# Kernel tuning notes

Measured on AMD Instinct MI355X. Metric: run time of the kernel, lower is better.

Reference implementation:

```python
import jax, jax.numpy as jnp
import numpy as np

B, N, H, NH = 8, 1024, 512, 8
HD = H // NH
SCALE = float(np.sqrt(HD))


def setup_inputs() -> dict:
    key = jax.random.key(0)
    ks = jax.random.split(key, 14)
    s = 0.02
    return {
        "x": jax.random.normal(ks[0], (B, N, H), jnp.float32),
        "distance_matrix": jax.random.uniform(ks[1], (B, N, N), jnp.float32),
        "mask": jax.random.randint(ks[2], (B, N), 0, 2).astype(bool),
        "Wq": jax.random.normal(ks[3], (H, H), jnp.float32) * s,
        "bq": jnp.zeros((H,), jnp.float32),
        "Wk": jax.random.normal(ks[4], (H, H), jnp.float32) * s,
        "bk": jnp.zeros((H,), jnp.float32),
        "Wv": jax.random.normal(ks[5], (H, H), jnp.float32) * s,
        "bv": jnp.zeros((H,), jnp.float32),
        "Wo": jax.random.normal(ks[6], (H, H), jnp.float32) * s,
        "bo": jnp.zeros((H,), jnp.float32),
        "dist_emb": jax.random.normal(ks[7], (50, NH), jnp.float32) * s,
        "attn_bias": jnp.zeros((NH, 1, 1), jnp.float32),
    }


def reference(x, distance_matrix, mask, Wq, bq, Wk, bk, Wv, bv, Wo, bo, dist_emb, attn_bias):
    Bb, Nn, _ = x.shape
    # projections (torch Linear: x @ W.T + b), split heads -> [B, N, NH, HD]
    Q = (x @ Wq.T + bq).reshape(Bb, Nn, NH, HD)
    K = (x @ Wk.T + bk).reshape(Bb, Nn, NH, HD)
    V = (x @ Wv.T + bv).reshape(Bb, Nn, NH, HD)
    # scores [B, NH, N, N]
    scores = jnp.einsum('bqhd,bkhd->bhqk', Q, K) / SCALE
    # distance-bin bias lookup: [B,N,N] -> bins -> [B,N,N,NH] -> [B,NH,N,N]
    bins = jnp.clip((distance_matrix * 10.0).astype(jnp.int32), 0, 49)
    dbias = jnp.transpose(dist_emb[bins], (0, 3, 1, 2))
    scores = scores + dbias + attn_bias[None]  # attn_bias [NH,1,1] broadcasts
    scores = jnp.where(mask[:, None, None, :], -1e9, scores)  # mask over keys
    attn = jax.nn.softmax(scores, axis=-1)  # dropout = identity in eval
    out = jnp.einsum('bhqk,bkhd->bqhd', attn, V).reshape(Bb, Nn, H)
    return out @ Wo.T + bo
```

## Files before the change

### kernel.cpp

```cpp
#include <hip/hip_runtime.h>
#include <hip/hip_bf16.h>
#include <math.h>

#define B_  8
#define N_  1024
#define H_  512
#define NH_ 8
#define HD_ 64

typedef __attribute__((ext_vector_type(8))) short short8;
typedef __attribute__((ext_vector_type(4))) short short4_t;
typedef __attribute__((ext_vector_type(4))) float floatx4;

#define GPTR(p) ((const __attribute__((address_space(1))) void*)(p))
#define LPTR(p) ((__attribute__((address_space(3))) void*)(p))

#define TRB16(dst, addr, IMM) \
    asm volatile("ds_read_b64_tr_b16 %0, %1 offset:" IMM \
                 : "=v"(dst) : "v"(addr) : "memory")

#define EXP2(x) exp2f(x)
#define LOG2E 1.44269504088896f

static __device__ __forceinline__ unsigned short f2bf(float f) {
    __hip_bfloat16 h = __float2bfloat16(f);
    unsigned short u;
    __builtin_memcpy(&u, &h, 2);
    return u;
}

__global__ __launch_bounds__(256) void prep_kernel(
    const float* __restrict__ x,  const float* __restrict__ wq,
    const float* __restrict__ wk, const float* __restrict__ wv,
    const float* __restrict__ wo, unsigned short* __restrict__ dst,
    const float* __restrict__ dist, const int* __restrict__ mask,
    unsigned char* __restrict__ bins)
{
    const int bid = blockIdx.x;
    if (bid < 1280) {
        const int n4 = (4194304 + 4 * 262144) / 4;
        int i = bid * 256 + threadIdx.x;
        for (; i < n4; i += 1280 * 256) {
            const int e = i * 4;
            const float* src;
            if (e < 4194304) {
                src = x + e;
            } else {
                const int rel = e - 4194304;
                const int w = rel >> 18;
                const int off = rel & 262143;
                src = (w == 0 ? wq : w == 1 ? wk : w == 2 ? wv : wo) + off;
            }
            const float4 v = *(const float4*)src;
            ushort4 r;
            r.x = f2bf(v.x); r.y = f2bf(v.y); r.z = f2bf(v.z); r.w = f2bf(v.w);
            *(ushort4*)(dst + e) = r;
        }
    } else {
        const int gid = (bid - 1280) * 256 + threadIdx.x;
        const size_t e = (size_t)gid * 16;
        const int b = gid >> 16;
        const int k = (gid & 63) * 16;
        const float* dsrc = dist + e;
        const int*   msrc = mask + b * N_ + k;
        unsigned w[4];
        #pragma unroll
        for (int i = 0; i < 4; ++i) {
            const float4 v = *(const float4*)(dsrc + 4 * i);
            const int4  mm = *(const int4*)(msrc + 4 * i);
            int b0 = (int)(v.x * 10.f); b0 = b0 < 0 ? 0 : (b0 > 49 ? 49 : b0);
            int b1 = (int)(v.y * 10.f); b1 = b1 < 0 ? 0 : (b1 > 49 ? 49 : b1);
            int b2 = (int)(v.z * 10.f); b2 = b2 < 0 ? 0 : (b2 > 49 ? 49 : b2);
            int b3 = (int)(v.w * 10.f); b3 = b3 < 0 ? 0 : (b3 > 49 ? 49 : b3);
            if (mm.x) b0 = 255;
            if (mm.y) b1 = 255;
            if (mm.z) b2 = 255;
            if (mm.w) b3 = 255;
            w[i] = (unsigned)b0 | ((unsigned)b1 << 8) | ((unsigned)b2 << 16) | ((unsigned)b3 << 24);
        }
        uint4 u; u.x = w[0]; u.y = w[1]; u.z = w[2]; u.w = w[3];
        *(uint4*)(bins + e) = u;
    }
}

template <int BF16OUT>
static __device__ __forceinline__ void gemm_core(
    const unsigned short* __restrict__ A, const unsigned short* __restrict__ W,
    const float* __restrict__ bias, void* __restrict__ C,
    int Ncols, int K, float scale, int row0, int col0)
{
    __shared__ unsigned short As[128 * 32];
    __shared__ unsigned short Bs[128 * 32];

    const int t    = threadIdx.x;
    const int lane = t & 63;
    const int wave = t >> 6;
    const int wr   = wave >> 1;
    const int wc   = wave & 1;
    const int l15  = lane & 15;
    const int lhi  = lane >> 4;

    const int srow = wave * 32 + (lane >> 2);
    const int sk   = (lane & 3) * 8;
    const unsigned short* gA = A + (size_t)(row0 + srow) * K + sk;
    const unsigned short* gB = W + (size_t)(col0 + srow) * K + sk;

    floatx4 acc[4][4];
    #pragma unroll
    for (int m = 0; m < 4; ++m)
        #pragma unroll
        for (int n = 0; n < 4; ++n) acc[m][n] = (floatx4)0.f;

    for (int k0 = 0; k0 < K; k0 += 32) {
        __syncthreads();
        #pragma unroll
        for (int i = 0; i < 2; ++i) {
            __builtin_amdgcn_global_load_lds(GPTR(gA + (size_t)(i * 16) * K + k0),
                                             LPTR(&As[(wave * 32 + i * 16) * 32]), 16, 0, 0);
            __builtin_amdgcn_global_load_lds(GPTR(gB + (size_t)(i * 16) * K + k0),
                                             LPTR(&Bs[(wave * 32 + i * 16) * 32]), 16, 0, 0);
        }
        __syncthreads();

        short8 af[4], bf[4];
        #pragma unroll
        for (int m = 0; m < 4; ++m)
            af[m] = *(const short8*)&As[(wr * 64 + m * 16 + l15) * 32 + lhi * 8];
        #pragma unroll
        for (int n = 0; n < 4; ++n)
            bf[n] = *(const short8*)&Bs[(wc * 64 + n * 16 + l15) * 32 + lhi * 8];
        #pragma unroll
        for (int m = 0; m < 4; ++m)
            #pragma unroll
            for (int n = 0; n < 4; ++n)
                acc[m][n] = __builtin_amdgcn_mfma_f32_16x16x32_bf16(af[m], bf[n], acc[m][n], 0, 0, 0);
    }

    #pragma unroll
    for (int n = 0; n < 4; ++n) {
        const int col = col0 + wc * 64 + n * 16 + l15;
        const float bvv = bias[col];
        #pragma unroll
        for (int m = 0; m < 4; ++m) {
            #pragma unroll
            for (int r = 0; r < 4; ++r) {
                const int row = row0 + wr * 64 + m * 16 + lhi * 4 + r;
                const float v = (acc[m][n][r] + bvv) * scale;
                if (BF16OUT)
                    ((unsigned short*)C)[(size_t)row * Ncols + col] = f2bf(v);
                else
                    ((float*)C)[(size_t)row * Ncols + col] = v;
            }
        }
    }
}

__global__ __launch_bounds__(256) void gemm_qkv(
    const unsigned short* __restrict__ xb,
    const unsigned short* __restrict__ Wq, const unsigned short* __restrict__ Wk,
    const unsigned short* __restrict__ Wv,
    const float* __restrict__ bq, const float* __restrict__ bk,
    const float* __restrict__ bv,
    unsigned short* __restrict__ Qb, unsigned short* __restrict__ Kb,
    unsigned short* __restrict__ Vb)
{
    const int z = blockIdx.z;
    const unsigned short* W = z == 0 ? Wq : (z == 1 ? Wk : Wv);
    const float* bias       = z == 0 ? bq : (z == 1 ? bk : bv);
    unsigned short* C       = z == 0 ? Qb : (z == 1 ? Kb : Vb);
    const float scale       = z == 0 ? (0.125f * LOG2E) : 1.0f;
    gemm_core<1>(xb, W, bias, C, H_, H_, scale, blockIdx.y * 128, blockIdx.x * 128);
}

__global__ __launch_bounds__(256) void gemm_out(
    const unsigned short* __restrict__ Ab, const unsigned short* __restrict__ Wo,
    const float* __restrict__ bo, float* __restrict__ out)
{
    gemm_core<0>(Ab, Wo, bo, out, H_, H_, 1.0f, blockIdx.y * 128, blockIdx.x * 128);
}

__global__ __launch_bounds__(256) void attn_mfma(
    const unsigned short* __restrict__ Qg, const unsigned short* __restrict__ Kg,
    const unsigned short* __restrict__ Vg, const unsigned char* __restrict__ bins,
    const float* __restrict__ demb, const float* __restrict__ abias,
    unsigned short* __restrict__ O)
{
    const int lin = blockIdx.x + 16 * blockIdx.y + 128 * blockIdx.z;
    const int swz = (lin & 7) * 128 + (lin >> 3);
    const int qt = swz & 15;
    const int h  = (swz >> 4) & 7;
    const int b  = swz >> 7;
    const int q0 = qt * 64;
    const int t  = threadIdx.x;
    const int lane = t & 63;
    const int wave = t >> 6;
    const int l15 = lane & 15;
    const int lhi = lane >> 4;

    __shared__ unsigned short Ks[64 * 64];
    __shared__ unsigned short Vs[64 * 64];
    __shared__ unsigned short QPs[64 * 64];
    __shared__ unsigned char  Bs[64 * 80];

    float dbl = -1.442695e9f;
    if (lane < 50) dbl = (demb[lane * NH_ + h] + abias[h]) * LOG2E;

    const unsigned short* ksrc[2];
    const unsigned short* vsrc[2];
    #pragma unroll
    for (int i = 0; i < 2; ++i) {
        const int C = wave * 128 + i * 64 + lane;
        const int kr = C >> 3, c = C & 7;
        ksrc[i] = Kg + ((size_t)(b * N_) + kr) * H_ + h * HD_ + ((c ^ (kr & 7)) * 8);
        const int vd16 = C >> 7, rem = C & 127;
        const int krhi = rem >> 3, r2 = rem & 7;
        const int vkr = krhi * 4 + (r2 >> 1), vc = r2 & 1;
        vsrc[i] = Vg + ((size_t)(b * N_) + vkr) * H_ + h * HD_ + vd16 * 16 + vc * 8;
    }
    const unsigned char* bsrc = bins + ((size_t)(b * N_) + q0 + (t >> 2)) * N_ + (t & 3) * 16;
    const int bidx = (t >> 2) * 80 + (t & 3) * 16;

    {
        const int qr = t >> 2;
        const int d0 = (t & 3) * 16;
        const unsigned short* src = Qg + ((size_t)(b * N_ + q0 + qr)) * H_ + h * HD_ + d0;
        #pragma unroll
        for (int cc = 0; cc < 2; ++cc) {
            const uint4 v = *(const uint4*)(src + 8 * cc);
            const int idx = (qr * 64 + d0 + 8 * cc) ^ ((qr & 7) << 3);
            *(uint4*)&QPs[idx] = v;
        }
    }
    __syncthreads();

    short8 aq[2];
    {
        const int qrow = (wave << 4) + l15;
        #pragma unroll
        for (int ck = 0; ck < 2; ++ck) {
            const int kb = lhi * 8 + 32 * ck;
            const int idx = (qrow * 64 + kb) ^ ((qrow & 7) << 3);
            aq[ck] = *(const short8*)&QPs[idx];
        }
    }
    __syncthreads();

    unsigned short* const Pw = &QPs[wave << 10];
    const unsigned trlane = (unsigned)(lhi << 8) + (unsigned)(l15 << 3);
    const unsigned vaddr = (unsigned)(size_t)LPTR(&Vs[0]) + trlane;

    float m = -INFINITY, lsum = 0.f;
    floatx4 o4[4];
    #pragma unroll
    for (int nd = 0; nd < 4; ++nd) o4[nd] = (floatx4)0.f;

    for (int k0 = 0; k0 < N_; k0 += 64) {
        __syncthreads();
        {
            const size_t koff = (size_t)k0;
            #pragma unroll
            for (int i = 0; i < 2; ++i) {
                __builtin_amdgcn_global_load_lds(GPTR(ksrc[i] + koff * H_),
                    LPTR(&Ks[(wave * 128 + i * 64) * 8]), 16, 0, 0);
                __builtin_amdgcn_global_load_lds(GPTR(vsrc[i] + koff * H_),
                    LPTR(&Vs[(wave * 128 + i * 64) * 8]), 16, 0, 0);
            }
            const uint4 brv = *(const uint4*)(bsrc + koff);
            *(uint4*)&Bs[bidx] = brv;
        }
        __syncthreads();

        floatx4 s4[4];
        __builtin_amdgcn_s_setprio(1);
        #pragma unroll
        for (int kn = 0; kn < 4; ++kn) {
            const int kcol = kn * 16 + l15;
            floatx4 acc = (floatx4)0.f;
            #pragma unroll
            for (int ck = 0; ck < 2; ++ck) {
                const int kb = lhi * 8 + 32 * ck;
                const int idx = (kcol * 64 + kb) ^ ((kcol & 7) << 3);
                const short8 bk = *(const short8*)&Ks[idx];
                acc = __builtin_amdgcn_mfma_f32_16x16x32_bf16(bk, aq[ck], acc, 0, 0, 0);
            }
            s4[kn] = acc;
        }
        __builtin_amdgcn_s_setprio(0);

        #pragma unroll
        for (int kn = 0; kn < 4; ++kn) {
            const unsigned bb =
                *(const unsigned*)&Bs[((wave << 4) + l15) * 80 + kn * 16 + (lhi << 2)];
            s4[kn][0] += __shfl(dbl, (int)(bb & 255u), 64);
            s4[kn][1] += __shfl(dbl, (int)((bb >> 8) & 255u), 64);
            s4[kn][2] += __shfl(dbl, (int)((bb >> 16) & 255u), 64);
            s4[kn][3] += __shfl(dbl, (int)(bb >> 24), 64);
        }

        {
            float mx = s4[0][0];
            #pragma unroll
            for (int kn = 0; kn < 4; ++kn)
                #pragma unroll
                for (int r = 0; r < 4; ++r) mx = fmaxf(mx, s4[kn][r]);
            mx = fmaxf(mx, __shfl_xor(mx, 16, 64));
            mx = fmaxf(mx, __shfl_xor(mx, 32, 64));
            const float mnew = fmaxf(m, mx);
            float ts = 0.f;
            #pragma unroll
            for (int kn = 0; kn < 4; ++kn)
                #pragma unroll
                for (int r = 0; r < 4; ++r) {
                    const float p = EXP2(s4[kn][r] - mnew);
                    s4[kn][r] = p;
                    ts += p;
                }
            ts += __shfl_xor(ts, 16, 64);
            ts += __shfl_xor(ts, 32, 64);
            const float alpha = EXP2(m - mnew);
            lsum = lsum * alpha + ts;
            m = mnew;
            #pragma unroll
            for (int r = 0; r < 4; ++r) {
                const float ar = __shfl(alpha, lhi * 4 + r, 64);
                #pragma unroll
                for (int nd = 0; nd < 4; ++nd) o4[nd][r] *= ar;
            }
        }

        #pragma unroll
        for (int kn = 0; kn < 4; ++kn) {
            short4_t pk;
            pk[0] = (short)f2bf(s4[kn][0]);
            pk[1] = (short)f2bf(s4[kn][1]);
            pk[2] = (short)f2bf(s4[kn][2]);
            pk[3] = (short)f2bf(s4[kn][3]);
            const int idx = (l15 * 64 + kn * 16 + (lhi << 2)) ^ ((l15 & 7) << 3);
            *(short4_t*)&Pw[idx] = pk;
        }

        short8 ap[2];
        #pragma unroll
        for (int ck = 0; ck < 2; ++ck) {
            const int idx = (l15 * 64 + ck * 32 + lhi * 8) ^ ((l15 & 7) << 3);
            ap[ck] = *(const short8*)&Pw[idx];
        }
        short4_t v0l[4], v0h[4], v1l[4], v1h[4];
        TRB16(v0l[0], vaddr, "0");    TRB16(v0h[0], vaddr, "128");
        TRB16(v0l[1], vaddr, "2048"); TRB16(v0h[1], vaddr, "2176");
        TRB16(v0l[2], vaddr, "4096"); TRB16(v0h[2], vaddr, "4224");
        TRB16(v0l[3], vaddr, "6144"); TRB16(v0h[3], vaddr, "6272");
        TRB16(v1l[0], vaddr, "1024"); TRB16(v1h[0], vaddr, "1152");
        TRB16(v1l[1], vaddr, "3072"); TRB16(v1h[1], vaddr, "3200");
        TRB16(v1l[2], vaddr, "5120"); TRB16(v1h[2], vaddr, "5248");
        TRB16(v1l[3], vaddr, "7168"); TRB16(v1h[3], vaddr, "7296");
        asm volatile("s_waitcnt lgkmcnt(0)" ::: "memory");
        __builtin_amdgcn_sched_barrier(0);

        __builtin_amdgcn_s_setprio(1);
        #pragma unroll
        for (int nd = 0; nd < 4; ++nd) {
            const short8 bv0 = __builtin_shufflevector(v0l[nd], v0h[nd], 0, 1, 2, 3, 4, 5, 6, 7);
            o4[nd] = __builtin_amdgcn_mfma_f32_16x16x32_bf16(ap[0], bv0, o4[nd], 0, 0, 0);
            const short8 bv1 = __builtin_shufflevector(v1l[nd], v1h[nd], 0, 1, 2, 3, 4, 5, 6, 7);
            o4[nd] = __builtin_amdgcn_mfma_f32_16x16x32_bf16(ap[1], bv1, o4[nd], 0, 0, 0);
        }
        __builtin_amdgcn_s_setprio(0);
    }

    float inv[4];
    #pragma unroll
    for (int r = 0; r < 4; ++r) inv[r] = 1.f / __shfl(lsum, lhi * 4 + r, 64);
    #pragma unroll
    for (int nd = 0; nd < 4; ++nd) {
        const int d = nd * 16 + l15;
        #pragma unroll
        for (int r = 0; r < 4; ++r) {
            const int q = q0 + (wave << 4) + lhi * 4 + r;
            O[((size_t)(b * N_ + q)) * H_ + h * HD_ + d] = f2bf(o4[nd][r] * inv[r]);
        }
    }
}

extern "C" void kernel_launch(void* const* d_in, const int* in_sizes, int n_in,
                              void* d_out, int out_size, void* d_ws, size_t ws_size,
                              hipStream_t stream)
{
    const float* x    = (const float*)d_in[0];
    const float* dist = (const float*)d_in[1];
    const int*   mask = (const int*)d_in[2];
    const float* Wq   = (const float*)d_in[3];
    const float* bq   = (const float*)d_in[4];
    const float* Wk   = (const float*)d_in[5];
    const float* bk   = (const float*)d_in[6];
    const float* Wv   = (const float*)d_in[7];
    const float* bv   = (const float*)d_in[8];
    const float* Wo   = (const float*)d_in[9];
    const float* bo   = (const float*)d_in[10];
    const float* demb = (const float*)d_in[11];
    const float* ab   = (const float*)d_in[12];
    float* out = (float*)d_out;

    const size_t mat = (size_t)B_ * N_ * H_;
    const size_t wsz = (size_t)H_ * H_;

    unsigned short* blob = (unsigned short*)d_ws;
    unsigned short* xb  = blob;
    unsigned short* Wqb = blob + mat;
    unsigned short* Wkb = Wqb + wsz;
    unsigned short* Wvb = Wkb + wsz;
    unsigned short* Wob = Wvb + wsz;
    unsigned short* Qb  = Wob + wsz;
    unsigned short* Kb  = Qb + mat;
    unsigned short* Vb  = Kb + mat;
    unsigned short* Ab  = Vb + mat;
    unsigned char*  binsb = (unsigned char*)(Ab + mat);

    const dim3 blk(256);

    hipLaunchKernelGGL(prep_kernel, dim3(3328), blk, 0, stream,
                       x, Wq, Wk, Wv, Wo, blob, dist, mask, binsb);

    const dim3 qgrid(H_ / 128, (B_ * N_) / 128, 3);
    hipLaunchKernelGGL(gemm_qkv, qgrid, blk, 0, stream,
                       xb, Wqb, Wkb, Wvb, bq, bk, bv, Qb, Kb, Vb);

    const dim3 agrid(N_ / 64, NH_, B_);
    hipLaunchKernelGGL(attn_mfma, agrid, blk, 0, stream,
                       Qb, Kb, Vb, binsb, demb, ab, Ab);

    const dim3 ogrid(H_ / 128, (B_ * N_) / 128, 1);
    hipLaunchKernelGGL(gemm_out, ogrid, blk, 0, stream, Ab, Wob, bo, out);
}
```

Baseline: 107.0 us.

## Double attention query tile to 128 rows with 512-thread blocks sharing K/V tiles

Each attention block now covers 128 query rows with eight waves instead of 64 rows with four, so every K/V tile staged in LDS is reused by twice as many queries. Each thread issues one async global-to-LDS load per K and V tile instead of two. Global K/V traffic is halved, but the grid has half as many blocks, LDS use per block grows, and occupancy may drop. The Q/P and bins staging is enlarged to match.

```diff
diff --git a/kernel.cpp b/kernel.cpp
--- a/kernel.cpp
+++ b/kernel.cpp
@@ -179,18 +179,18 @@
     gemm_core<0>(Ab, Wo, bo, out, H_, H_, 1.0f, blockIdx.y * 128, blockIdx.x * 128);
 }
 
-__global__ __launch_bounds__(256) void attn_mfma(
+__global__ __launch_bounds__(512) void attn_mfma(
     const unsigned short* __restrict__ Qg, const unsigned short* __restrict__ Kg,
     const unsigned short* __restrict__ Vg, const unsigned char* __restrict__ bins,
     const float* __restrict__ demb, const float* __restrict__ abias,
     unsigned short* __restrict__ O)
 {
-    const int lin = blockIdx.x + 16 * blockIdx.y + 128 * blockIdx.z;
-    const int swz = (lin & 7) * 128 + (lin >> 3);
-    const int qt = swz & 15;
-    const int h  = (swz >> 4) & 7;
-    const int b  = swz >> 7;
-    const int q0 = qt * 64;
+    const int lin = blockIdx.x + 8 * blockIdx.y + 64 * blockIdx.z;
+    const int swz = (lin & 7) * 64 + (lin >> 3);
+    const int qt = swz & 7;
+    const int h  = (swz >> 3) & 7;
+    const int b  = swz >> 6;
+    const int q0 = qt * 128;
     const int t  = threadIdx.x;
     const int lane = t & 63;
     const int wave = t >> 6;
@@ -199,24 +199,21 @@
 
     __shared__ unsigned short Ks[64 * 64];
     __shared__ unsigned short Vs[64 * 64];
-    __shared__ unsigned short QPs[64 * 64];
-    __shared__ unsigned char  Bs[64 * 80];
+    __shared__ unsigned short QPs[128 * 64];
+    __shared__ unsigned char  Bs[128 * 80];
 
     float dbl = -1.442695e9f;
     if (lane < 50) dbl = (demb[lane * NH_ + h] + abias[h]) * LOG2E;
 
-    const unsigned short* ksrc[2];
-    const unsigned short* vsrc[2];
-    #pragma unroll
-    for (int i = 0; i < 2; ++i) {
-        const int C = wave * 128 + i * 64 + lane;
-        const int kr = C >> 3, c = C & 7;
-        ksrc[i] = Kg + ((size_t)(b * N_) + kr) * H_ + h * HD_ + ((c ^ (kr & 7)) * 8);
-        const int vd16 = C >> 7, rem = C & 127;
-        const int krhi = rem >> 3, r2 = rem & 7;
-        const int vkr = krhi * 4 + (r2 >> 1), vc = r2 & 1;
-        vsrc[i] = Vg + ((size_t)(b * N_) + vkr) * H_ + h * HD_ + vd16 * 16 + vc * 8;
-    }
+    const int C = wave * 64 + lane;
+    const int kr = C >> 3, kc = C & 7;
+    const unsigned short* ksrc =
+        Kg + ((size_t)(b * N_) + kr) * H_ + h * HD_ + ((kc ^ (kr & 7)) * 8);
+    const int vd16 = C >> 7, vrem = C & 127;
+    const int vkrhi = vrem >> 3, vr2 = vrem & 7;
+    const int vkr = vkrhi * 4 + (vr2 >> 1), vcc = vr2 & 1;
+    const unsigned short* vsrc =
+        Vg + ((size_t)(b * N_) + vkr) * H_ + h * HD_ + vd16 * 16 + vcc * 8;
     const unsigned char* bsrc = bins + ((size_t)(b * N_) + q0 + (t >> 2)) * N_ + (t & 3) * 16;
     const int bidx = (t >> 2) * 80 + (t & 3) * 16;
 
@@ -258,13 +255,10 @@
         __syncthreads();
         {
             const size_t koff = (size_t)k0;
-            #pragma unroll
-            for (int i = 0; i < 2; ++i) {
-                __builtin_amdgcn_global_load_lds(GPTR(ksrc[i] + koff * H_),
-                    LPTR(&Ks[(wave * 128 + i * 64) * 8]), 16, 0, 0);
-                __builtin_amdgcn_global_load_lds(GPTR(vsrc[i] + koff * H_),
-                    LPTR(&Vs[(wave * 128 + i * 64) * 8]), 16, 0, 0);
-            }
+            __builtin_amdgcn_global_load_lds(GPTR(ksrc + koff * H_),
+                LPTR(&Ks[(wave * 64) * 8]), 16, 0, 0);
+            __builtin_amdgcn_global_load_lds(GPTR(vsrc + koff * H_),
+                LPTR(&Vs[(wave * 64) * 8]), 16, 0, 0);
             const uint4 brv = *(const uint4*)(bsrc + koff);
             *(uint4*)&Bs[bidx] = brv;
         }
@@ -425,8 +419,8 @@
     hipLaunchKernelGGL(gemm_qkv, qgrid, blk, 0, stream,
                        xb, Wqb, Wkb, Wvb, bq, bk, bv, Qb, Kb, Vb);
 
-    const dim3 agrid(N_ / 64, NH_, B_);
-    hipLaunchKernelGGL(attn_mfma, agrid, blk, 0, stream,
+    const dim3 agrid(N_ / 128, NH_, B_);
+    hipLaunchKernelGGL(attn_mfma, agrid, dim3(512), 0, stream,
                        Qb, Kb, Vb, binsb, demb, ab, Ab);
 
     const dim3 ogrid(H_ / 128, (B_ * N_) / 128, 1);
```

Measured after the change: 103.2 us. -3.6%, faster.
